# Optimization experiments

Hardware: AMD Instinct MI355X
Metric: run time of the kernel (lower is better)

Reference implementation:

```python
import jax, jax.numpy as jnp
import numpy as np

N = 50000      # nodes
E = 500000     # edges
IN = 128       # input feature dim
HID = 64       # hidden per-head dim
CLS = 64       # num classes
SLOPE = 0.2    # leaky_relu negative slope


def _gat_layer(x, W, al, ar, src, dst):
    """One GATConv: project, per-edge score, edge-softmax over dst, weighted aggregate.
    x: [N, Din], W: [Din, H*F], al/ar: [H, F]. Returns [N, H, F]."""
    H, F = al.shape
    n = x.shape[0]
    feat = (x @ W).reshape(n, H, F)                      # [N,H,F]
    el = jnp.einsum('nhf,hf->nh', feat, al)              # [N,H]
    er = jnp.einsum('nhf,hf->nh', feat, ar)              # [N,H]
    e = el[src] + er[dst]                                # u_add_v -> [E,H]
    e = jnp.where(e >= 0, e, SLOPE * e)                  # leaky_relu
    # edge_softmax over destination nodes (numerically stable)
    m = jax.lax.stop_gradient(jax.ops.segment_max(e, dst, num_segments=n))
    ex = jnp.exp(e - m[dst])
    denom = jax.ops.segment_sum(ex, dst, num_segments=n)
    a = ex / denom[dst]                                  # [E,H]
    # u_mul_e + sum aggregation
    out = jax.ops.segment_sum(feat[src] * a[:, :, None], dst, num_segments=n)
    return out                                           # [N,H,F]


def setup_inputs() -> dict:
    key = jax.random.key(0)
    ks = jax.random.split(key, 12)
    s = 0.05  # xavier-ish scale
    x = jax.random.normal(ks[0], (N, IN), jnp.float32)
    src = jax.random.randint(ks[1], (E,), 0, N)
    dst = jax.random.randint(ks[2], (E,), 0, N)
    W1 = jax.random.normal(ks[3], (IN, 4 * HID), jnp.float32) * s
    al1 = jax.random.normal(ks[4], (4, HID), jnp.float32) * s
    ar1 = jax.random.normal(ks[5], (4, HID), jnp.float32) * s
    W2 = jax.random.normal(ks[6], (4 * HID, 4 * HID), jnp.float32) * s
    al2 = jax.random.normal(ks[7], (4, HID), jnp.float32) * s
    ar2 = jax.random.normal(ks[8], (4, HID), jnp.float32) * s
    W3 = jax.random.normal(ks[9], (4 * HID, CLS), jnp.float32) * s
    al3 = jax.random.normal(ks[10], (1, CLS), jnp.float32) * s
    ar3 = jax.random.normal(ks[11], (1, CLS), jnp.float32) * s
    res_W3 = jax.random.normal(jax.random.fold_in(key, 99), (4 * HID, CLS), jnp.float32) * s
    return {"x": x, "W1": W1, "al1": al1, "ar1": ar1, "W2": W2, "al2": al2,
            "ar2": ar2, "W3": W3, "al3": al3, "ar3": ar3, "res_W3": res_W3,
            "src": src, "dst": dst}


def reference(x, W1, al1, ar1, W2, al2, ar2, W3, al3, ar3, res_W3, src, dst):
    # layer 0: no residual, elu activation, flatten heads
    h = _gat_layer(x, W1, al1, ar1, src, dst)            # [N,4,64]
    h = jax.nn.elu(h).reshape(N, -1)                     # [N,256]
    # layer 1: residual is Identity (in_dst 256 == 4*64), elu, flatten
    h1 = _gat_layer(h, W2, al2, ar2, src, dst)           # [N,4,64]
    h1 = h1 + h.reshape(N, 4, HID)                       # residual (Identity)
    h = jax.nn.elu(h1).reshape(N, -1)                    # [N,256]
    # layer 2: residual Linear 256->64, no activation, mean over heads
    h2 = _gat_layer(h, W3, al3, ar3, src, dst)           # [N,1,64]
    h2 = h2 + (h @ res_W3).reshape(N, 1, CLS)            # residual fc
    logits = h2.mean(axis=1)                             # [N,64]
    return logits
```

## Files before the change

### kernel.cpp

```cpp
#include <hip/hip_runtime.h>
#include <hip/hip_bf16.h>
#include <math.h>

#define SLOPE 0.2f

typedef __attribute__((ext_vector_type(8))) short short8;
typedef __attribute__((ext_vector_type(4))) float f32x4;

static __device__ __forceinline__ float leakyf(float x) { return x >= 0.f ? x : SLOPE * x; }
static __device__ __forceinline__ float bflo(unsigned u) { return __builtin_bit_cast(float, u << 16); }
static __device__ __forceinline__ float bfhi(unsigned u) { return __builtin_bit_cast(float, u & 0xffff0000u); }
static __device__ __forceinline__ unsigned short f2bf(float f) {
    unsigned u = __builtin_bit_cast(unsigned, f);
    return (unsigned short)((u + 0x7fff + ((u >> 16) & 1)) >> 16);
}

struct __align__(8) us4 { unsigned short a, b, c, d; };

__global__ void tconv(const float* __restrict__ W, unsigned short* __restrict__ Wt, int K, int Nc) {
    int i = blockIdx.x * blockDim.x + threadIdx.x;
    if (i < K * Nc) {
        int k = i / Nc, n = i - k * Nc;
        Wt[(size_t)n * K + k] = f2bf(W[i]);
    }
}

template<bool A_F32>
__global__ __launch_bounds__(256) void gemm_l12(const void* __restrict__ Av,
                                                const unsigned short* __restrict__ Wt,
                                                unsigned short* __restrict__ outb,
                                                const float* __restrict__ al,
                                                const float* __restrict__ ar,
                                                float* __restrict__ el,
                                                float* __restrict__ er,
                                                int M, int K) {
    const int lane = threadIdx.x & 63;
    const int wid = threadIdx.x >> 6;
    const int rlo = lane & 15;
    const int q = lane >> 4;
    const int kg = q * 8;
    const int m0 = blockIdx.x * 64;
    const int cbase = wid * 64;

    f32x4 acc[4][4];
#pragma unroll
    for (int mf = 0; mf < 4; ++mf)
#pragma unroll
        for (int nf = 0; nf < 4; ++nf) acc[mf][nf] = (f32x4){0.f, 0.f, 0.f, 0.f};

    for (int k0 = 0; k0 < K; k0 += 32) {
        short8 a[4];
#pragma unroll
        for (int mf = 0; mf < 4; ++mf) {
            int r = m0 + mf * 16 + rlo;
            if (r >= M) r = M - 1;
            if (A_F32) {
                const float* ap = (const float*)Av + (size_t)r * K + k0 + kg;
                float4 f0 = *(const float4*)ap;
                float4 f1 = *(const float4*)(ap + 4);
                short8 t;
                t[0] = f2bf(f0.x); t[1] = f2bf(f0.y); t[2] = f2bf(f0.z); t[3] = f2bf(f0.w);
                t[4] = f2bf(f1.x); t[5] = f2bf(f1.y); t[6] = f2bf(f1.z); t[7] = f2bf(f1.w);
                a[mf] = t;
            } else {
                a[mf] = *(const short8*)((const unsigned short*)Av + (size_t)r * K + k0 + kg);
            }
        }
#pragma unroll
        for (int nf = 0; nf < 4; ++nf) {
            short8 b = *(const short8*)(Wt + (size_t)(cbase + nf * 16 + rlo) * K + k0 + kg);
#pragma unroll
            for (int mf = 0; mf < 4; ++mf)
                acc[mf][nf] = __builtin_amdgcn_mfma_f32_16x16x32_bf16(a[mf], b, acc[mf][nf], 0, 0, 0);
        }
    }

    float alv[4], arv[4];
#pragma unroll
    for (int nf = 0; nf < 4; ++nf) {
        alv[nf] = al[cbase + nf * 16 + rlo];
        arv[nf] = ar[cbase + nf * 16 + rlo];
    }

#pragma unroll
    for (int mf = 0; mf < 4; ++mf) {
#pragma unroll
        for (int reg = 0; reg < 4; ++reg) {
            int r = m0 + mf * 16 + q * 4 + reg;
            float pl = 0.f, pr = 0.f;
#pragma unroll
            for (int nf = 0; nf < 4; ++nf) {
                pl += acc[mf][nf][reg] * alv[nf];
                pr += acc[mf][nf][reg] * arv[nf];
            }
#pragma unroll
            for (int off = 1; off < 16; off <<= 1) {
                pl += __shfl_xor(pl, off);
                pr += __shfl_xor(pr, off);
            }
            if (rlo == 0 && r < M) {
                el[(size_t)r * 4 + wid] = pl;
                er[(size_t)r * 4 + wid] = pr;
            }
            if (r < M) {
#pragma unroll
                for (int nf = 0; nf < 4; ++nf)
                    outb[(size_t)r * 256 + cbase + nf * 16 + rlo] = f2bf(acc[mf][nf][reg]);
            }
        }
    }
}

__global__ __launch_bounds__(256) void gemm_l3(const unsigned short* __restrict__ A,
                                               const unsigned short* __restrict__ Wt,
                                               unsigned short* __restrict__ featb,
                                               float* __restrict__ resf,
                                               const float* __restrict__ al,
                                               const float* __restrict__ ar,
                                               float* __restrict__ el,
                                               float* __restrict__ er, int M) {
    const int K = 256;
    const int lane = threadIdx.x & 63;
    const int wid = threadIdx.x >> 6;
    const int rlo = lane & 15;
    const int q = lane >> 4;
    const int kg = q * 8;
    const int m0 = blockIdx.x * 128 + (wid >> 1) * 64;
    const int ch = wid & 1;
    const int cbase = ch * 64;

    f32x4 acc[4][4];
#pragma unroll
    for (int mf = 0; mf < 4; ++mf)
#pragma unroll
        for (int nf = 0; nf < 4; ++nf) acc[mf][nf] = (f32x4){0.f, 0.f, 0.f, 0.f};

    for (int k0 = 0; k0 < K; k0 += 32) {
        short8 a[4];
#pragma unroll
        for (int mf = 0; mf < 4; ++mf) {
            int r = m0 + mf * 16 + rlo;
            if (r >= M) r = M - 1;
            a[mf] = *(const short8*)(A + (size_t)r * K + k0 + kg);
        }
#pragma unroll
        for (int nf = 0; nf < 4; ++nf) {
            short8 b = *(const short8*)(Wt + (size_t)(cbase + nf * 16 + rlo) * K + k0 + kg);
#pragma unroll
            for (int mf = 0; mf < 4; ++mf)
                acc[mf][nf] = __builtin_amdgcn_mfma_f32_16x16x32_bf16(a[mf], b, acc[mf][nf], 0, 0, 0);
        }
    }

    float alv[4], arv[4];
    if (ch == 0) {
#pragma unroll
        for (int nf = 0; nf < 4; ++nf) {
            alv[nf] = al[nf * 16 + rlo];
            arv[nf] = ar[nf * 16 + rlo];
        }
    }

#pragma unroll
    for (int mf = 0; mf < 4; ++mf) {
#pragma unroll
        for (int reg = 0; reg < 4; ++reg) {
            int r = m0 + mf * 16 + q * 4 + reg;
            if (ch == 0) {
                float pl = 0.f, pr = 0.f;
#pragma unroll
                for (int nf = 0; nf < 4; ++nf) {
                    pl += acc[mf][nf][reg] * alv[nf];
                    pr += acc[mf][nf][reg] * arv[nf];
                }
#pragma unroll
                for (int off = 1; off < 16; off <<= 1) {
                    pl += __shfl_xor(pl, off);
                    pr += __shfl_xor(pr, off);
                }
                if (rlo == 0 && r < M) { el[r] = pl; er[r] = pr; }
                if (r < M) {
#pragma unroll
                    for (int nf = 0; nf < 4; ++nf)
                        featb[(size_t)r * 64 + nf * 16 + rlo] = f2bf(acc[mf][nf][reg]);
                }
            } else if (r < M) {
#pragma unroll
                for (int nf = 0; nf < 4; ++nf)
                    resf[(size_t)r * 64 + nf * 16 + rlo] = acc[mf][nf][reg];
            }
        }
    }
}

__global__ void hist_kernel(const int* __restrict__ dst, int* __restrict__ counts, int e) {
    int i = blockIdx.x * blockDim.x + threadIdx.x;
    if (i < e) atomicAdd(&counts[dst[i]], 1);
}

__global__ __launch_bounds__(1024) void scan_block(const int* __restrict__ counts,
                                                   int* __restrict__ offsets,
                                                   int* __restrict__ bsums, int n) {
    __shared__ int ws[16];
    int tid = threadIdx.x, lane = tid & 63, wid = tid >> 6;
    int idx = blockIdx.x * 1024 + tid;
    int v = (idx < n) ? counts[idx] : 0;
    int s = v;
#pragma unroll
    for (int off = 1; off < 64; off <<= 1) {
        int t = __shfl_up(s, off);
        if (lane >= off) s += t;
    }
    if (lane == 63) ws[wid] = s;
    __syncthreads();
    if (tid < 16) {
        int w2 = ws[tid];
#pragma unroll
        for (int off = 1; off < 16; off <<= 1) {
            int t = __shfl_up(w2, off);
            if (tid >= off) w2 += t;
        }
        ws[tid] = w2;
    }
    __syncthreads();
    int wpre = wid ? ws[wid - 1] : 0;
    if (idx < n) offsets[idx] = wpre + s - v;
    if (tid == 0) bsums[blockIdx.x] = ws[15];
}

__global__ void scan_sums(int* bsums, int nb) {
    int lane = threadIdx.x;
    int v = (lane < nb) ? bsums[lane] : 0;
    int s = v;
#pragma unroll
    for (int off = 1; off < 64; off <<= 1) {
        int t = __shfl_up(s, off);
        if (lane >= off) s += t;
    }
    if (lane < nb) bsums[lane] = s - v;
}

__global__ __launch_bounds__(1024) void add_off(const int* __restrict__ bsums,
                                                int* __restrict__ offsets,
                                                int* __restrict__ cursor, int n, int e) {
    int idx = blockIdx.x * 1024 + threadIdx.x;
    if (idx < n) {
        int v = offsets[idx] + bsums[blockIdx.x];
        offsets[idx] = v;
        cursor[idx] = v;
    }
    if (idx == 0) offsets[n] = e;
}

__global__ void scatter_kernel(const int* __restrict__ src, const int* __restrict__ dst,
                               int* __restrict__ cursor, int* __restrict__ csr_src, int e) {
    int i = blockIdx.x * blockDim.x + threadIdx.x;
    if (i < e) {
        int pos = atomicAdd(&cursor[dst[i]], 1);
        csr_src[pos] = src[i];
    }
}

template<int H, int RES, int ACT, bool OUT_BF16>
__global__ __launch_bounds__(256) void gat_agg(const unsigned short* __restrict__ fp,
                                               const float* __restrict__ el,
                                               const float* __restrict__ er,
                                               const int* __restrict__ offsets,
                                               const int* __restrict__ csr_src,
                                               const void* __restrict__ resid,
                                               void* __restrict__ outv, int n) {
    const int D = H * 64;
    int node = blockIdx.x * 4 + (threadIdx.x >> 6);
    int lane = threadIdx.x & 63;
    if (node >= n) return;
    int e0 = offsets[node], e1 = offsets[node + 1];
    const int head = (H == 4) ? (lane >> 4) : 0;
    float erh = er[(size_t)node * H + head];

    float denA = 0.f, denB = 0.f;
    float accA[4] = {0.f, 0.f, 0.f, 0.f};
    float accB[4] = {0.f, 0.f, 0.f, 0.f};

#define STEP(DEN, AC, LV, UX, UY)                                      \
    {                                                                  \
        float xx = fminf(leakyf((LV) + erh), 80.f);                    \
        float w = __expf(xx);                                          \
        DEN += w;                                                      \
        AC[0] += w * bflo(UX);                                         \
        if (H == 4) {                                                  \
            AC[1] += w * bfhi(UX);                                     \
            AC[2] += w * bflo(UY);                                     \
            AC[3] += w * bfhi(UY);                                     \
        }                                                              \
    }

    int e = e0;
    for (; e + 4 <= e1; e += 4) {
        int s0 = csr_src[e], s1 = csr_src[e + 1], s2 = csr_src[e + 2], s3 = csr_src[e + 3];
        float l0 = el[(size_t)s0 * H + head];
        float l1 = el[(size_t)s1 * H + head];
        float l2 = el[(size_t)s2 * H + head];
        float l3 = el[(size_t)s3 * H + head];
        unsigned x0, y0 = 0, x1, y1 = 0, x2, y2 = 0, x3, y3 = 0;
        if (H == 4) {
            uint2 u0 = *(const uint2*)(fp + (size_t)s0 * D + lane * 4);
            uint2 u1 = *(const uint2*)(fp + (size_t)s1 * D + lane * 4);
            uint2 u2 = *(const uint2*)(fp + (size_t)s2 * D + lane * 4);
            uint2 u3 = *(const uint2*)(fp + (size_t)s3 * D + lane * 4);
            x0 = u0.x; y0 = u0.y; x1 = u1.x; y1 = u1.y;
            x2 = u2.x; y2 = u2.y; x3 = u3.x; y3 = u3.y;
        } else {
            x0 = fp[(size_t)s0 * D + lane];
            x1 = fp[(size_t)s1 * D + lane];
            x2 = fp[(size_t)s2 * D + lane];
            x3 = fp[(size_t)s3 * D + lane];
        }
        STEP(denA, accA, l0, x0, y0);
        STEP(denB, accB, l1, x1, y1);
        STEP(denA, accA, l2, x2, y2);
        STEP(denB, accB, l3, x3, y3);
    }
    for (; e < e1; ++e) {
        int s0 = csr_src[e];
        float l0 = el[(size_t)s0 * H + head];
        unsigned x0, y0 = 0;
        if (H == 4) {
            uint2 u0 = *(const uint2*)(fp + (size_t)s0 * D + lane * 4);
            x0 = u0.x; y0 = u0.y;
        } else {
            x0 = fp[(size_t)s0 * D + lane];
        }
        STEP(denA, accA, l0, x0, y0);
    }
#undef STEP

    float den = denA + denB;
    float inv = den > 0.f ? 1.f / den : 0.f;
    float v[4];
#pragma unroll
    for (int i = 0; i < 4; ++i) v[i] = (accA[i] + accB[i]) * inv;

    if (RES == 1) {
        uint2 ru = *(const uint2*)((const unsigned short*)resid + (size_t)node * D + lane * 4);
        v[0] += bflo(ru.x); v[1] += bfhi(ru.x); v[2] += bflo(ru.y); v[3] += bfhi(ru.y);
    } else if (RES == 2) {
        v[0] += ((const float*)resid)[(size_t)node * D + lane];
    }
    if (ACT == 1) {
#pragma unroll
        for (int i = 0; i < 4; ++i) v[i] = v[i] > 0.f ? v[i] : __expf(v[i]) - 1.f;
    }
    if (OUT_BF16) {
        if (H == 4) {
            us4 o = {f2bf(v[0]), f2bf(v[1]), f2bf(v[2]), f2bf(v[3])};
            *(us4*)((unsigned short*)outv + (size_t)node * D + lane * 4) = o;
        } else {
            ((unsigned short*)outv)[(size_t)node * D + lane] = f2bf(v[0]);
        }
    } else {
        if (H == 4) {
            float4 o = {v[0], v[1], v[2], v[3]};
            *(float4*)((float*)outv + (size_t)node * D + lane * 4) = o;
        } else {
            ((float*)outv)[(size_t)node * D + lane] = v[0];
        }
    }
}

extern "C" void kernel_launch(void* const* d_in, const int* in_sizes, int n_in,
                              void* d_out, int out_size, void* d_ws, size_t ws_size,
                              hipStream_t stream) {
    const float* x      = (const float*)d_in[0];
    const float* W1     = (const float*)d_in[1];
    const float* al1    = (const float*)d_in[2];
    const float* ar1    = (const float*)d_in[3];
    const float* W2     = (const float*)d_in[4];
    const float* al2    = (const float*)d_in[5];
    const float* ar2    = (const float*)d_in[6];
    const float* W3     = (const float*)d_in[7];
    const float* al3    = (const float*)d_in[8];
    const float* ar3    = (const float*)d_in[9];
    const float* res_W3 = (const float*)d_in[10];
    const int*   src    = (const int*)d_in[11];
    const int*   dst    = (const int*)d_in[12];

    const int N = in_sizes[0] / 128;
    const int E = in_sizes[11];

    float* out = (float*)d_out;

    unsigned short* featb = (unsigned short*)d_ws;
    unsigned short* h1    = featb + (size_t)N * 256;
    unsigned short* h2    = h1 + (size_t)N * 256;
    unsigned short* W1t   = h2 + (size_t)N * 256;
    unsigned short* W2t   = W1t + 256 * 128;
    unsigned short* W3c   = W2t + 256 * 256;
    float* resf = (float*)(W3c + 128 * 256);
    float* el   = resf + (size_t)N * 64;
    float* er   = el + (size_t)N * 4;
    int* offsets = (int*)(er + (size_t)N * 4);
    int* cursor  = offsets + (N + 1);
    int* csr_src = cursor + N;
    int* bsums   = csr_src + E;

    const int T = 256;
    const int scan_blocks = (N + 1023) / 1024;

    tconv<<<(128 * 256 + T - 1) / T, T, 0, stream>>>(W1, W1t, 128, 256);
    tconv<<<(256 * 256 + T - 1) / T, T, 0, stream>>>(W2, W2t, 256, 256);
    tconv<<<(256 * 64 + T - 1) / T, T, 0, stream>>>(W3, W3c, 256, 64);
    tconv<<<(256 * 64 + T - 1) / T, T, 0, stream>>>(res_W3, W3c + 64 * 256, 256, 64);

    hipMemsetAsync(cursor, 0, (size_t)N * sizeof(int), stream);
    hist_kernel<<<(E + T - 1) / T, T, 0, stream>>>(dst, cursor, E);
    scan_block<<<scan_blocks, 1024, 0, stream>>>(cursor, offsets, bsums, N);
    scan_sums<<<1, 64, 0, stream>>>(bsums, scan_blocks);
    add_off<<<scan_blocks, 1024, 0, stream>>>(bsums, offsets, cursor, N, E);
    scatter_kernel<<<(E + T - 1) / T, T, 0, stream>>>(src, dst, cursor, csr_src, E);

    int gemm12_blocks = (N + 63) / 64;
    int gemm3_blocks = (N + 127) / 128;
    int node_blocks = (N + 3) / 4;

    gemm_l12<true><<<gemm12_blocks, T, 0, stream>>>(x, W1t, featb, al1, ar1, el, er, N, 128);
    gat_agg<4, 0, 1, true><<<node_blocks, T, 0, stream>>>(featb, el, er, offsets, csr_src, nullptr, h1, N);

    gemm_l12<false><<<gemm12_blocks, T, 0, stream>>>(h1, W2t, featb, al2, ar2, el, er, N, 256);
    gat_agg<4, 1, 1, true><<<node_blocks, T, 0, stream>>>(featb, el, er, offsets, csr_src, h1, h2, N);

    gemm_l3<<<gemm3_blocks, T, 0, stream>>>(h2, W3c, featb, resf, al3, ar3, el, er, N);
    gat_agg<1, 2, 0, false><<<node_blocks, T, 0, stream>>>(featb, el, er, offsets, csr_src, resf, out, N);
}
```

Measured before the change: 291.7 us.

## Cooperatively compute edge weights per chunk and merge small setup kernels

The aggregation kernel now computes attention weights for a chunk of edges in parallel across lanes, one edge-head pair per lane. It stages the weights and source ids in LDS, then walks the chunk to gather features, so each lane no longer runs the redundant per-edge el loads and exp. Separately, the four weight-transpose launches are merged into one kernel. The scan_sums kernel is also folded into add_off, with each block reducing the preceding block sums itself. These cut launch count and redundant transcendental work, but add LDS traffic. The wave-local LDS handoff depends only on an lgkmcnt wait rather than a barrier.

```diff
diff --git a/kernel.cpp b/kernel.cpp
--- a/kernel.cpp
+++ b/kernel.cpp
@@ -17,12 +17,21 @@
 
 struct __align__(8) us4 { unsigned short a, b, c, d; };
 
-__global__ void tconv(const float* __restrict__ W, unsigned short* __restrict__ Wt, int K, int Nc) {
-    int i = blockIdx.x * blockDim.x + threadIdx.x;
-    if (i < K * Nc) {
-        int k = i / Nc, n = i - k * Nc;
-        Wt[(size_t)n * K + k] = f2bf(W[i]);
-    }
+__global__ __launch_bounds__(256) void tconv_all(const float* __restrict__ W1,
+                                                 const float* __restrict__ W2,
+                                                 const float* __restrict__ W3,
+                                                 const float* __restrict__ rW3,
+                                                 unsigned short* __restrict__ W1t,
+                                                 unsigned short* __restrict__ W2t,
+                                                 unsigned short* __restrict__ W3c) {
+    int i = blockIdx.x * 256 + threadIdx.x;
+    const float* W; unsigned short* Wt; int K, lNc, idx;
+    if (i < 32768)       { W = W1;  Wt = W1t;            K = 128; lNc = 8; idx = i; }
+    else if (i < 98304)  { W = W2;  Wt = W2t;            K = 256; lNc = 8; idx = i - 32768; }
+    else if (i < 114688) { W = W3;  Wt = W3c;            K = 256; lNc = 6; idx = i - 98304; }
+    else                 { W = rW3; Wt = W3c + 64 * 256; K = 256; lNc = 6; idx = i - 114688; }
+    int k = idx >> lNc, n = idx & ((1 << lNc) - 1);
+    Wt[n * K + k] = f2bf(W[idx]);
 }
 
 template<bool A_F32>
@@ -228,24 +237,21 @@
     if (tid == 0) bsums[blockIdx.x] = ws[15];
 }
 
-__global__ void scan_sums(int* bsums, int nb) {
-    int lane = threadIdx.x;
-    int v = (lane < nb) ? bsums[lane] : 0;
-    int s = v;
-#pragma unroll
-    for (int off = 1; off < 64; off <<= 1) {
-        int t = __shfl_up(s, off);
-        if (lane >= off) s += t;
-    }
-    if (lane < nb) bsums[lane] = s - v;
-}
-
 __global__ __launch_bounds__(1024) void add_off(const int* __restrict__ bsums,
                                                 int* __restrict__ offsets,
-                                                int* __restrict__ cursor, int n, int e) {
-    int idx = blockIdx.x * 1024 + threadIdx.x;
+                                                int* __restrict__ cursor, int n, int e, int nb) {
+    __shared__ int base_s;
+    int tid = threadIdx.x;
+    if (tid < 64) {
+        int v = (tid < blockIdx.x && tid < nb) ? bsums[tid] : 0;
+#pragma unroll
+        for (int off = 32; off > 0; off >>= 1) v += __shfl_xor(v, off);
+        if (tid == 0) base_s = v;
+    }
+    __syncthreads();
+    int idx = blockIdx.x * 1024 + tid;
     if (idx < n) {
-        int v = offsets[idx] + bsums[blockIdx.x];
+        int v = offsets[idx] + base_s;
         offsets[idx] = v;
         cursor[idx] = v;
     }
@@ -270,75 +276,77 @@
                                                const void* __restrict__ resid,
                                                void* __restrict__ outv, int n) {
     const int D = H * 64;
+    const int CH = (H == 4) ? 16 : 64;
+    __shared__ float lw[4][64];
+    __shared__ int ls[4][64];
     int node = blockIdx.x * 4 + (threadIdx.x >> 6);
     int lane = threadIdx.x & 63;
+    int wv = threadIdx.x >> 6;
     if (node >= n) return;
     int e0 = offsets[node], e1 = offsets[node + 1];
-    const int head = (H == 4) ? (lane >> 4) : 0;
-    float erh = er[(size_t)node * H + head];
-
-    float denA = 0.f, denB = 0.f;
-    float accA[4] = {0.f, 0.f, 0.f, 0.f};
-    float accB[4] = {0.f, 0.f, 0.f, 0.f};
-
-#define STEP(DEN, AC, LV, UX, UY)                                      \
-    {                                                                  \
-        float xx = fminf(leakyf((LV) + erh), 80.f);                    \
-        float w = __expf(xx);                                          \
-        DEN += w;                                                      \
-        AC[0] += w * bflo(UX);                                         \
-        if (H == 4) {                                                  \
-            AC[1] += w * bfhi(UX);                                     \
-            AC[2] += w * bflo(UY);                                     \
-            AC[3] += w * bfhi(UY);                                     \
-        }                                                              \
-    }
+    const int hs = (H == 4) ? (lane & 3) : 0;
+    const int hf = (H == 4) ? (lane >> 4) : 0;
+    const int js = (H == 4) ? (lane >> 2) : lane;
+    float er_s = er[(size_t)node * H + hs];
+
+    float den = 0.f;
+    float acc[4] = {0.f, 0.f, 0.f, 0.f};
 
     int e = e0;
-    for (; e + 4 <= e1; e += 4) {
-        int s0 = csr_src[e], s1 = csr_src[e + 1], s2 = csr_src[e + 2], s3 = csr_src[e + 3];
-        float l0 = el[(size_t)s0 * H + head];
-        float l1 = el[(size_t)s1 * H + head];
-        float l2 = el[(size_t)s2 * H + head];
-        float l3 = el[(size_t)s3 * H + head];
-        unsigned x0, y0 = 0, x1, y1 = 0, x2, y2 = 0, x3, y3 = 0;
-        if (H == 4) {
-            uint2 u0 = *(const uint2*)(fp + (size_t)s0 * D + lane * 4);
-            uint2 u1 = *(const uint2*)(fp + (size_t)s1 * D + lane * 4);
-            uint2 u2 = *(const uint2*)(fp + (size_t)s2 * D + lane * 4);
-            uint2 u3 = *(const uint2*)(fp + (size_t)s3 * D + lane * 4);
-            x0 = u0.x; y0 = u0.y; x1 = u1.x; y1 = u1.y;
-            x2 = u2.x; y2 = u2.y; x3 = u3.x; y3 = u3.y;
-        } else {
-            x0 = fp[(size_t)s0 * D + lane];
-            x1 = fp[(size_t)s1 * D + lane];
-            x2 = fp[(size_t)s2 * D + lane];
-            x3 = fp[(size_t)s3 * D + lane];
-        }
-        STEP(denA, accA, l0, x0, y0);
-        STEP(denB, accB, l1, x1, y1);
-        STEP(denA, accA, l2, x2, y2);
-        STEP(denB, accB, l3, x3, y3);
-    }
-    for (; e < e1; ++e) {
-        int s0 = csr_src[e];
-        float l0 = el[(size_t)s0 * H + head];
-        unsigned x0, y0 = 0;
-        if (H == 4) {
-            uint2 u0 = *(const uint2*)(fp + (size_t)s0 * D + lane * 4);
-            x0 = u0.x; y0 = u0.y;
-        } else {
-            x0 = fp[(size_t)s0 * D + lane];
-        }
-        STEP(denA, accA, l0, x0, y0);
-    }
-#undef STEP
-
-    float den = denA + denB;
+    while (e < e1) {
+        int cnt = e1 - e;
+        if (cnt > CH) cnt = CH;
+        float w = 0.f;
+        int s = 0;
+        if (js < cnt) {
+            s = csr_src[e + js];
+            float xx = fminf(leakyf(el[(size_t)s * H + hs] + er_s), 80.f);
+            w = __expf(xx);
+        }
+        lw[wv][lane] = w;
+        if (H == 4) { if (hs == 0) ls[wv][js] = s; }
+        else ls[wv][lane] = s;
+        asm volatile("s_waitcnt lgkmcnt(0)" ::: "memory");
+
+        int j = 0;
+        for (; j + 2 <= cnt; j += 2) {
+            float w0 = lw[wv][(H == 4) ? (j * 4 + hf) : j];
+            float w1 = lw[wv][(H == 4) ? ((j + 1) * 4 + hf) : (j + 1)];
+            int s0 = ls[wv][j], s1 = ls[wv][j + 1];
+            den += w0 + w1;
+            if (H == 4) {
+                uint2 u0 = *(const uint2*)(fp + (size_t)s0 * D + lane * 4);
+                uint2 u1 = *(const uint2*)(fp + (size_t)s1 * D + lane * 4);
+                acc[0] += w0 * bflo(u0.x) + w1 * bflo(u1.x);
+                acc[1] += w0 * bfhi(u0.x) + w1 * bfhi(u1.x);
+                acc[2] += w0 * bflo(u0.y) + w1 * bflo(u1.y);
+                acc[3] += w0 * bfhi(u0.y) + w1 * bfhi(u1.y);
+            } else {
+                acc[0] += w0 * bflo((unsigned)fp[(size_t)s0 * D + lane])
+                        + w1 * bflo((unsigned)fp[(size_t)s1 * D + lane]);
+            }
+        }
+        if (j < cnt) {
+            float w0 = lw[wv][(H == 4) ? (j * 4 + hf) : j];
+            int s0 = ls[wv][j];
+            den += w0;
+            if (H == 4) {
+                uint2 u0 = *(const uint2*)(fp + (size_t)s0 * D + lane * 4);
+                acc[0] += w0 * bflo(u0.x);
+                acc[1] += w0 * bfhi(u0.x);
+                acc[2] += w0 * bflo(u0.y);
+                acc[3] += w0 * bfhi(u0.y);
+            } else {
+                acc[0] += w0 * bflo((unsigned)fp[(size_t)s0 * D + lane]);
+            }
+        }
+        e += cnt;
+    }
+
     float inv = den > 0.f ? 1.f / den : 0.f;
     float v[4];
 #pragma unroll
-    for (int i = 0; i < 4; ++i) v[i] = (accA[i] + accB[i]) * inv;
+    for (int i = 0; i < 4; ++i) v[i] = acc[i] * inv;
 
     if (RES == 1) {
         uint2 ru = *(const uint2*)((const unsigned short*)resid + (size_t)node * D + lane * 4);
@@ -406,16 +414,12 @@
     const int T = 256;
     const int scan_blocks = (N + 1023) / 1024;
 
-    tconv<<<(128 * 256 + T - 1) / T, T, 0, stream>>>(W1, W1t, 128, 256);
-    tconv<<<(256 * 256 + T - 1) / T, T, 0, stream>>>(W2, W2t, 256, 256);
-    tconv<<<(256 * 64 + T - 1) / T, T, 0, stream>>>(W3, W3c, 256, 64);
-    tconv<<<(256 * 64 + T - 1) / T, T, 0, stream>>>(res_W3, W3c + 64 * 256, 256, 64);
+    tconv_all<<<512, T, 0, stream>>>(W1, W2, W3, res_W3, W1t, W2t, W3c);
 
     hipMemsetAsync(cursor, 0, (size_t)N * sizeof(int), stream);
     hist_kernel<<<(E + T - 1) / T, T, 0, stream>>>(dst, cursor, E);
     scan_block<<<scan_blocks, 1024, 0, stream>>>(cursor, offsets, bsums, N);
-    scan_sums<<<1, 64, 0, stream>>>(bsums, scan_blocks);
-    add_off<<<scan_blocks, 1024, 0, stream>>>(bsums, offsets, cursor, N, E);
+    add_off<<<scan_blocks, 1024, 0, stream>>>(bsums, offsets, cursor, N, E, scan_blocks);
     scatter_kernel<<<(E + T - 1) / T, T, 0, stream>>>(src, dst, cursor, csr_src, E);
 
     int gemm12_blocks = (N + 63) / 64;
```

Result: faster. 284.9 us (-2.3%).
